# Optimization experiments

Measured on AMD Instinct MI355X. Metric: run time of the kernel, lower is better.

Reference implementation:

```python
import jax, jax.numpy as jnp
import numpy as np

N_NODES = 100000
HIDDEN = 64
N_LAYERS = 4
N_EDGES = 800000
EPS = 1e-5  # equinox RMSNorm default


def rmsnorm(x, w):
    # per-node RMSNorm over last dim, learned scale, no bias
    inv = jax.lax.rsqrt(jnp.mean(x * x, axis=-1, keepdims=True) + EPS)
    return x * inv * w


def setup_inputs() -> dict:
    key = jax.random.key(0)
    ks = jax.random.split(key, 5)
    x = jax.random.normal(ks[0], (N_NODES, HIDDEN), dtype=jnp.float32)
    # eqx Linear weight (out,in), init ~ U(-1/sqrt(in), 1/sqrt(in)); randn*scale is fine for a baseline
    scale = 1.0 / np.sqrt(HIDDEN)
    conv_w = jax.random.normal(ks[1], (N_LAYERS, HIDDEN, HIDDEN), dtype=jnp.float32) * scale
    hid_w = jax.random.normal(ks[2], (N_LAYERS, HIDDEN, HIDDEN), dtype=jnp.float32) * scale
    conv_norm_w = jnp.ones((N_LAYERS, HIDDEN), dtype=jnp.float32)
    hid_norm_w = jnp.ones((N_LAYERS, HIDDEN), dtype=jnp.float32)
    row = jax.random.randint(ks[3], (N_EDGES,), 0, N_NODES, dtype=jnp.int32)
    col = jax.random.randint(ks[4], (N_EDGES,), 0, N_NODES, dtype=jnp.int32)
    return {"x": x, "conv_w": conv_w, "conv_norm_w": conv_norm_w,
            "hid_w": hid_w, "hid_norm_w": hid_norm_w, "row": row, "col": col}


def reference(x, conv_w, conv_norm_w, hid_w, hid_norm_w, row, col):
    n_nodes = x.shape[0]

    def step(h, params):
        cw, cnw, hw, hnw = params
        # GConvLayer: linear (no bias) -> relu -> sparse adjacency aggregation -> residual RMSNorm
        m = jax.nn.relu(h @ cw.T)                                  # [n_nodes, d]
        agg = jax.ops.segment_sum(m[col], row, num_segments=n_nodes)  # a @ m (unweighted COO)
        h = rmsnorm(h + agg, cnw)
        # HiddenLayer: linear -> relu -> residual RMSNorm
        y = jax.nn.relu(h @ hw.T)
        h = rmsnorm(h + y, hnw)
        return h, None

    x, _ = jax.lax.scan(step, x, (conv_w, conv_norm_w, hid_w, hid_norm_w))
    return x
```

## Files before the change

kernel.cpp:

```cpp
#include <hip/hip_runtime.h>
#include <hip/hip_bf16.h>

#define HIDDEN 64
#define EPS 1e-5f
#define NPB 64
#define WST 72

typedef __attribute__((ext_vector_type(8))) short bf16x8;
typedef __attribute__((ext_vector_type(4))) float f32x4;

__device__ __forceinline__ unsigned short f2b(float x) {
    __hip_bfloat16 b = __float2bfloat16(x);
    return *(unsigned short*)&b;
}
__device__ __forceinline__ float b2f(unsigned short u) {
    unsigned int ui = (unsigned int)u << 16;
    return *(float*)&ui;
}
__device__ __forceinline__ float b2f_lo(unsigned int u) { unsigned int ui = u << 16; return *(float*)&ui; }
__device__ __forceinline__ float b2f_hi(unsigned int u) { unsigned int ui = u & 0xffff0000u; return *(float*)&ui; }
__device__ __forceinline__ unsigned int pk2(float a, float b) {
    return (unsigned int)f2b(a) | ((unsigned int)f2b(b) << 16);
}


__global__ __launch_bounds__(256) void hist_rank_kernel(const int* __restrict__ row,
                                                        int* __restrict__ cnt,
                                                        int* __restrict__ erank, int e) {
    int stride = gridDim.x * blockDim.x;
    for (int i = blockIdx.x * blockDim.x + threadIdx.x; i < e; i += stride) {
        int r = row[i];
        erank[i] = atomicAdd(&cnt[r], 1);
    }
}

__global__ __launch_bounds__(256) void block_sum_kernel(const int* __restrict__ cnt,
                                                        int* __restrict__ bsum, int n) {
    __shared__ int wsum[4];
    int tid = threadIdx.x;
    int i = blockIdx.x * 256 + tid;
    int v = (i < n) ? cnt[i] : 0;
#pragma unroll
    for (int off = 32; off > 0; off >>= 1) v += __shfl_xor(v, off, 64);
    if ((tid & 63) == 0) wsum[tid >> 6] = v;
    __syncthreads();
    if (tid == 0) bsum[blockIdx.x] = wsum[0] + wsum[1] + wsum[2] + wsum[3];
}

__global__ __launch_bounds__(256) void scan_final_kernel(const int* __restrict__ cnt,
                                                         const int* __restrict__ bsum,
                                                         int* __restrict__ row_ptr,
                                                         int n, int nb) {
    __shared__ int wred[4];
    __shared__ int wsum[4];
    __shared__ int wexcl[4];
    __shared__ int s_prev;
    __shared__ int s_tot;
    int b = blockIdx.x;
    int tid = threadIdx.x;
    int lane = tid & 63;
    int w = tid >> 6;
    int acc = 0;
    for (int j = tid; j < b; j += 256) acc += bsum[j];
#pragma unroll
    for (int off = 32; off > 0; off >>= 1) acc += __shfl_xor(acc, off, 64);
    if (lane == 0) wred[w] = acc;
    int i = b * 256 + tid;
    int v = (i < n) ? cnt[i] : 0;
    int sc = v;
#pragma unroll
    for (int off = 1; off < 64; off <<= 1) {
        int t = __shfl_up(sc, off, 64);
        if (lane >= off) sc += t;
    }
    if (lane == 63) wsum[w] = sc;
    __syncthreads();
    if (tid == 0) {
        s_prev = wred[0] + wred[1] + wred[2] + wred[3];
        int a = 0;
#pragma unroll
        for (int j = 0; j < 4; j++) { wexcl[j] = a; a += wsum[j]; }
        s_tot = a;
    }
    __syncthreads();
    if (i < n) row_ptr[i] = s_prev + wexcl[w] + (sc - v);
    if (b == nb - 1 && tid == 0) row_ptr[n] = s_prev + s_tot;
}

__global__ __launch_bounds__(256) void fill_kernel(const int* __restrict__ row,
                                                   const int* __restrict__ col,
                                                   const int* __restrict__ row_ptr,
                                                   const int* __restrict__ erank,
                                                   int* __restrict__ ecol, int e, int n) {
    int cls = blockIdx.x & 7;
    int sub = blockIdx.x >> 3;
    int nsub = gridDim.x >> 3;
    int lo = (int)(((long long)n * cls) >> 3);
    int hi = (int)(((long long)n * (cls + 1)) >> 3);
    for (int i = sub * 256 + threadIdx.x; i < e; i += nsub * 256) {
        int r = row[i];
        if (r >= lo && r < hi) {
            int pos = row_ptr[r] + erank[i];
            ecol[pos] = col[i];
        }
    }
}

__global__ __launch_bounds__(256) void wconv_kernel(const float* __restrict__ cw,
                                                    const float* __restrict__ hw,
                                                    unsigned short* __restrict__ wbt, int L) {
    int idx = blockIdx.x * blockDim.x + threadIdx.x;
    int total = 2 * L * 4096;
    if (idx >= total) return;
    int mat = idx >> 12;
    int rem = idx & 4095;
    const float* src = (mat < L) ? (cw + (size_t)mat * 4096) : (hw + (size_t)(mat - L) * 4096);
    wbt[idx] = f2b(src[rem]);
}


__device__ __forceinline__ void mfma_tile(const unsigned short* s_a,
                                          const unsigned short* s_b,
                                          int l16, int quad, int wbase, f32x4 acc[4]) {
    const unsigned short* ap = &s_a[(size_t)(wbase + l16) * WST + quad * 8];
    const unsigned short* bp = &s_b[(size_t)l16 * WST + quad * 8];
#pragma unroll
    for (int kt = 0; kt < 2; kt++) {
        bf16x8 a = *(const bf16x8*)(ap + kt * 32);
#pragma unroll
        for (int nt = 0; nt < 4; nt++) {
            bf16x8 b = *(const bf16x8*)(bp + (size_t)nt * 16 * WST + kt * 32);
            acc[nt] = __builtin_amdgcn_mfma_f32_16x16x32_bf16(a, b, acc[nt], 0, 0, 0);
        }
    }
}

__device__ __forceinline__ void stage_wb(const unsigned short* __restrict__ wsrc,
                                         unsigned short* s_wb, int tid) {
    for (int i = tid; i < 512; i += 256) {
        int r = i >> 3, seg = i & 7;
        *(uint4*)(&s_wb[r * WST + seg * 8]) = ((const uint4*)(wsrc + r * 64))[seg];
    }
}

__device__ __forceinline__ void acc8(float* p, uint4 u, bool ok) {
    p[0] += ok ? b2f_lo(u.x) : 0.f;
    p[1] += ok ? b2f_hi(u.x) : 0.f;
    p[2] += ok ? b2f_lo(u.y) : 0.f;
    p[3] += ok ? b2f_hi(u.y) : 0.f;
    p[4] += ok ? b2f_lo(u.z) : 0.f;
    p[5] += ok ? b2f_hi(u.z) : 0.f;
    p[6] += ok ? b2f_lo(u.w) : 0.f;
    p[7] += ok ? b2f_hi(u.w) : 0.f;
}


__global__ __launch_bounds__(256) void mm_relu_kernel(const float* __restrict__ h,
                                                      const unsigned short* __restrict__ wb,
                                                      __hip_bfloat16* __restrict__ m, int n) {
    __shared__ unsigned short s_hb[NPB * WST];
    __shared__ unsigned short s_wb[64 * WST];
    int tid = threadIdx.x;
    int base = blockIdx.x * NPB;
    stage_wb(wb, s_wb, tid);
    for (int i = tid; i < 512; i += 256) {
        int r = i >> 3, seg = i & 7;
        if (base + r < n) {
            const float4* hp = (const float4*)(h + (size_t)(base + r) * HIDDEN + seg * 8);
            float4 ha = hp[0], hb = hp[1];
            uint4 p;
            p.x = pk2(ha.x, ha.y);
            p.y = pk2(ha.z, ha.w);
            p.z = pk2(hb.x, hb.y);
            p.w = pk2(hb.z, hb.w);
            *(uint4*)(&s_hb[r * WST + seg * 8]) = p;
        } else {
            *(uint4*)(&s_hb[r * WST + seg * 8]) = make_uint4(0u, 0u, 0u, 0u);
        }
    }
    __syncthreads();
    int lane = tid & 63, wave = tid >> 6;
    int quad = lane >> 4, l16 = lane & 15;
    int wbase = wave * 16;
    f32x4 acc[4];
    acc[0] = (f32x4){0.f,0.f,0.f,0.f}; acc[1] = (f32x4){0.f,0.f,0.f,0.f};
    acc[2] = (f32x4){0.f,0.f,0.f,0.f}; acc[3] = (f32x4){0.f,0.f,0.f,0.f};
    mfma_tile(s_hb, s_wb, l16, quad, wbase, acc);
    unsigned short* mo = (unsigned short*)m;
#pragma unroll
    for (int r = 0; r < 4; r++) {
        int node = base + wbase + quad * 4 + r;
        if (node < n) {
#pragma unroll
            for (int nt = 0; nt < 4; nt++)
                mo[(size_t)node * HIDDEN + nt * 16 + l16] = f2b(fmaxf(acc[nt][r], 0.f));
        }
    }
}


__global__ __launch_bounds__(256) void fused_layer_kernel(
        const float* hf, const __hip_bfloat16* hb_in,
        const __hip_bfloat16* __restrict__ m_in,
        const unsigned short* __restrict__ hwb,
        const unsigned short* cwb_next,
        const int* __restrict__ row_ptr, const int* __restrict__ ecol,
        const float* __restrict__ cnw, const float* __restrict__ hnw,
        float* out_f32, __hip_bfloat16* hb_new, __hip_bfloat16* m_out, int n) {
    __shared__ unsigned short s_hb[NPB * WST];
    __shared__ unsigned short s_wb[64 * WST];
    int tid = threadIdx.x;
    int base = blockIdx.x * NPB;
    int lane = tid & 63, wave = tid >> 6;

    stage_wb(hwb, s_wb, tid);

    int g = lane >> 2;
    int sl = lane & 3;
    int gb = lane & ~3;
    int nl = wave * 16 + g;
    int node = base + nl;

    const float4* cp = (const float4*)(cnw + 16 * sl);
    float4 c0 = cp[0], c1 = cp[1], c2 = cp[2], c3 = cp[3];
    const unsigned short* mi = (const unsigned short*)m_in;

    uint4 q0 = make_uint4(0u, 0u, 0u, 0u);
    uint4 q1 = make_uint4(0u, 0u, 0u, 0u);
    if (node < n) {
        float p[16];
        if (hf) {
            const float4* hp = (const float4*)(hf + (size_t)node * HIDDEN + 16 * sl);
            float4 v0 = hp[0], v1 = hp[1], v2 = hp[2], v3 = hp[3];
            p[0]=v0.x;  p[1]=v0.y;  p[2]=v0.z;  p[3]=v0.w;
            p[4]=v1.x;  p[5]=v1.y;  p[6]=v1.z;  p[7]=v1.w;
            p[8]=v2.x;  p[9]=v2.y;  p[10]=v2.z; p[11]=v2.w;
            p[12]=v3.x; p[13]=v3.y; p[14]=v3.z; p[15]=v3.w;
        } else {
            const uint4* hp = (const uint4*)((const unsigned short*)hb_in + (size_t)node * HIDDEN + 16 * sl);
            uint4 u0 = hp[0], u1 = hp[1];
            p[0]=b2f_lo(u0.x);  p[1]=b2f_hi(u0.x);
            p[2]=b2f_lo(u0.y);  p[3]=b2f_hi(u0.y);
            p[4]=b2f_lo(u0.z);  p[5]=b2f_hi(u0.z);
            p[6]=b2f_lo(u0.w);  p[7]=b2f_hi(u0.w);
            p[8]=b2f_lo(u1.x);  p[9]=b2f_hi(u1.x);
            p[10]=b2f_lo(u1.y); p[11]=b2f_hi(u1.y);
            p[12]=b2f_lo(u1.z); p[13]=b2f_hi(u1.z);
            p[14]=b2f_lo(u1.w); p[15]=b2f_hi(u1.w);
        }
        int beg = row_ptr[node];
        int end = row_ptr[node + 1];
        int myc = 0;
        if (beg < end) {
            int idx = beg + sl;
            myc = ecol[idx < end ? idx : end - 1];
        }
        for (int b0 = beg; b0 < end; b0 += 4) {
            int nxt = b0 + 4;
            int nmyc = 0;
            if (nxt < end) {
                int idx = nxt + sl;
                nmyc = ecol[idx < end ? idx : end - 1];
            }
            int cnt = end - b0;
            if (cnt > 4) cnt = 4;
            int cj[4];
#pragma unroll
            for (int j = 0; j < 4; j++) cj[j] = __shfl(myc, gb + j, 64);
            uint4 ua[4], ub[4];
#pragma unroll
            for (int j = 0; j < 4; j++) {
                const uint4* mp = (const uint4*)(mi + (size_t)cj[j] * HIDDEN + 16 * sl);
                ua[j] = mp[0];
                ub[j] = mp[1];
            }
#pragma unroll
            for (int j = 0; j < 4; j++) {
                bool ok = j < cnt;
                acc8(p, ua[j], ok);
                acc8(p + 8, ub[j], ok);
            }
            myc = nmyc;
        }
        float ss = 0.f;
#pragma unroll
        for (int k = 0; k < 16; k++) ss += p[k] * p[k];
        ss += __shfl_xor(ss, 1, 64);
        ss += __shfl_xor(ss, 2, 64);
        float inv = rsqrtf(ss * (1.0f / 64.0f) + EPS);
        q0.x = pk2(p[0]*inv*c0.x,  p[1]*inv*c0.y);
        q0.y = pk2(p[2]*inv*c0.z,  p[3]*inv*c0.w);
        q0.z = pk2(p[4]*inv*c1.x,  p[5]*inv*c1.y);
        q0.w = pk2(p[6]*inv*c1.z,  p[7]*inv*c1.w);
        q1.x = pk2(p[8]*inv*c2.x,  p[9]*inv*c2.y);
        q1.y = pk2(p[10]*inv*c2.z, p[11]*inv*c2.w);
        q1.z = pk2(p[12]*inv*c3.x, p[13]*inv*c3.y);
        q1.w = pk2(p[14]*inv*c3.z, p[15]*inv*c3.w);
    }
    *(uint4*)(&s_hb[(size_t)nl * WST + 16 * sl]) = q0;
    *(uint4*)(&s_hb[(size_t)nl * WST + 16 * sl + 8]) = q1;
    __syncthreads();

    int quad = lane >> 4, l16 = lane & 15;
    int wbase = wave * 16;
    f32x4 acc[4];
    acc[0] = (f32x4){0.f,0.f,0.f,0.f}; acc[1] = (f32x4){0.f,0.f,0.f,0.f};
    acc[2] = (f32x4){0.f,0.f,0.f,0.f}; acc[3] = (f32x4){0.f,0.f,0.f,0.f};
    mfma_tile(s_hb, s_wb, l16, quad, wbase, acc);

    float hv[4][4];
    float ssq[4] = {0.f, 0.f, 0.f, 0.f};
#pragma unroll
    for (int r = 0; r < 4; r++) {
        int nr = wbase + quad * 4 + r;
#pragma unroll
        for (int nt = 0; nt < 4; nt++) {
            float hres = b2f(s_hb[(size_t)nr * WST + nt * 16 + l16]);
            float v = hres + fmaxf(acc[nt][r], 0.f);
            hv[r][nt] = v;
            ssq[r] += v * v;
        }
    }
#pragma unroll
    for (int mk = 1; mk <= 8; mk <<= 1) {
#pragma unroll
        for (int r = 0; r < 4; r++) ssq[r] += __shfl_xor(ssq[r], mk, 64);
    }
    float nwv[4];
#pragma unroll
    for (int nt = 0; nt < 4; nt++) nwv[nt] = hnw[nt * 16 + l16];
#pragma unroll
    for (int r = 0; r < 4; r++) {
        float inv = rsqrtf(ssq[r] * (1.0f / 64.0f) + EPS);
#pragma unroll
        for (int nt = 0; nt < 4; nt++) hv[r][nt] *= inv * nwv[nt];
    }
    if (out_f32) {
#pragma unroll
        for (int r = 0; r < 4; r++) {
            int nd = base + wbase + quad * 4 + r;
            if (nd < n) {
#pragma unroll
                for (int nt = 0; nt < 4; nt++)
                    out_f32[(size_t)nd * HIDDEN + nt * 16 + l16] = hv[r][nt];
            }
        }
    }
    if (hb_new) {
        unsigned short* ho = (unsigned short*)hb_new;
#pragma unroll
        for (int r = 0; r < 4; r++) {
            int nd = base + wbase + quad * 4 + r;
            if (nd < n) {
#pragma unroll
                for (int nt = 0; nt < 4; nt++)
                    ho[(size_t)nd * HIDDEN + nt * 16 + l16] = f2b(hv[r][nt]);
            }
        }
    }

    if (!m_out) return;

    bf16x8 wf[8];
    {
        const unsigned short* wp = cwb_next + (size_t)l16 * 64 + quad * 8;
#pragma unroll
        for (int nt = 0; nt < 4; nt++) {
#pragma unroll
            for (int kt = 0; kt < 2; kt++)
                wf[nt * 2 + kt] = *(const bf16x8*)(wp + (size_t)nt * 16 * 64 + kt * 32);
        }
    }

#pragma unroll
    for (int r = 0; r < 4; r++) {
        int nr = wbase + quad * 4 + r;
#pragma unroll
        for (int nt = 0; nt < 4; nt++)
            s_hb[(size_t)nr * WST + nt * 16 + l16] = f2b(hv[r][nt]);
    }

    f32x4 acc2[4];
    acc2[0] = (f32x4){0.f,0.f,0.f,0.f}; acc2[1] = (f32x4){0.f,0.f,0.f,0.f};
    acc2[2] = (f32x4){0.f,0.f,0.f,0.f}; acc2[3] = (f32x4){0.f,0.f,0.f,0.f};
    {
        const unsigned short* ap = &s_hb[(size_t)(wbase + l16) * WST + quad * 8];
#pragma unroll
        for (int kt = 0; kt < 2; kt++) {
            bf16x8 a = *(const bf16x8*)(ap + kt * 32);
#pragma unroll
            for (int nt = 0; nt < 4; nt++)
                acc2[nt] = __builtin_amdgcn_mfma_f32_16x16x32_bf16(a, wf[nt * 2 + kt], acc2[nt], 0, 0, 0);
        }
    }
    unsigned short* mo = (unsigned short*)m_out;
#pragma unroll
    for (int r = 0; r < 4; r++) {
        int nd = base + wbase + quad * 4 + r;
        if (nd < n) {
#pragma unroll
            for (int nt = 0; nt < 4; nt++)
                mo[(size_t)nd * HIDDEN + nt * 16 + l16] = f2b(fmaxf(acc2[nt][r], 0.f));
        }
    }
}


static inline size_t align_up(size_t x, size_t a) { return (x + a - 1) & ~(a - 1); }

extern "C" void kernel_launch(void* const* d_in, const int* in_sizes, int n_in,
                              void* d_out, int out_size, void* d_ws, size_t ws_size,
                              hipStream_t stream) {
    const float* x       = (const float*)d_in[0];
    const float* conv_w  = (const float*)d_in[1];
    const float* conv_nw = (const float*)d_in[2];
    const float* hid_w   = (const float*)d_in[3];
    const float* hid_nw  = (const float*)d_in[4];
    const int*   row     = (const int*)d_in[5];
    const int*   col     = (const int*)d_in[6];
    float* out = (float*)d_out;

    const int n = in_sizes[0] / HIDDEN;
    const int e = in_sizes[5];
    const int L = in_sizes[1] / 4096;

    size_t off = 0;
    char* ws = (char*)d_ws;
    __hip_bfloat16* mA = (__hip_bfloat16*)(ws + off);  off = align_up(off + (size_t)n * HIDDEN * 2, 16);
    __hip_bfloat16* mB = (__hip_bfloat16*)(ws + off);  off = align_up(off + (size_t)n * HIDDEN * 2, 16);
    __hip_bfloat16* hb1 = (__hip_bfloat16*)(ws + off); off = align_up(off + (size_t)n * HIDDEN * 2, 16);
    __hip_bfloat16* hb2 = (__hip_bfloat16*)(ws + off); off = align_up(off + (size_t)n * HIDDEN * 2, 16);
    unsigned short* wbt = (unsigned short*)(ws + off); off = align_up(off + (size_t)2 * L * 4096 * 2, 16);
    int* row_ptr = (int*)(ws + off);           off = align_up(off + (size_t)(n + 1) * 4, 16);
    int* cnt = (int*)(ws + off);               off = align_up(off + (size_t)n * 4, 16);
    int* bsum = (int*)(ws + off);              off = align_up(off + (size_t)1024 * 4, 16);
    int* erank = (int*)(ws + off);             off = align_up(off + (size_t)e * 4, 16);
    int* ecol = (int*)(ws + off);              off = align_up(off + (size_t)e * 4, 16);

    const int nb = (n + 255) / 256;

    hipMemsetAsync(cnt, 0, (size_t)n * 4, stream);
    hist_rank_kernel<<<1024, 256, 0, stream>>>(row, cnt, erank, e);
    block_sum_kernel<<<nb, 256, 0, stream>>>(cnt, bsum, n);
    scan_final_kernel<<<nb, 256, 0, stream>>>(cnt, bsum, row_ptr, n, nb);
    fill_kernel<<<1024, 256, 0, stream>>>(row, col, row_ptr, erank, ecol, e, n);

    wconv_kernel<<<(2 * L * 4096 + 255) / 256, 256, 0, stream>>>(conv_w, hid_w, wbt, L);

    const int blocks = (n + NPB - 1) / NPB;

    mm_relu_kernel<<<blocks, 256, 0, stream>>>(x, wbt, mA, n);

    const __hip_bfloat16* mi = mA;
    __hip_bfloat16* mo = mB;
    __hip_bfloat16* hin = nullptr;
    __hip_bfloat16* hout = hb1;
    for (int l = 0; l < L; l++) {
        bool last = (l == L - 1);
        fused_layer_kernel<<<blocks, 256, 0, stream>>>(
            (l == 0) ? x : nullptr, hin, mi,
            wbt + (size_t)(L + l) * 4096,
            last ? nullptr : (wbt + (size_t)(l + 1) * 4096),
            row_ptr, ecol,
            conv_nw + (size_t)l * HIDDEN, hid_nw + (size_t)l * HIDDEN,
            last ? out : nullptr,
            last ? nullptr : hout,
            last ? nullptr : mo, n);
        __hip_bfloat16* tmp = (__hip_bfloat16*)mi; mi = mo; mo = tmp;
        hin = hout;
        hout = (hout == hb1) ? hb2 : hb1;
    }
}
```

Before: 291.0 us.

## Drop LDS weight staging and block barrier; use 128-thread blocks in fused layer

Measured after the change: 291.9 us. No clear change (+0.3%).

```diff
diff --git a/kernel.cpp b/kernel.cpp
--- a/kernel.cpp
+++ b/kernel.cpp
@@ -4,6 +4,7 @@
 #define HIDDEN 64
 #define EPS 1e-5f
 #define NPB 64
+#define FNPB 32
 #define WST 72
 
 typedef __attribute__((ext_vector_type(8))) short bf16x8;
@@ -132,6 +133,17 @@
             bf16x8 b = *(const bf16x8*)(bp + (size_t)nt * 16 * WST + kt * 32);
             acc[nt] = __builtin_amdgcn_mfma_f32_16x16x32_bf16(a, b, acc[nt], 0, 0, 0);
         }
+    }
+}
+
+__device__ __forceinline__ void load_wfrag(const unsigned short* __restrict__ w,
+                                           int l16, int quad, bf16x8 wf[8]) {
+    const unsigned short* wp = w + (size_t)l16 * 64 + quad * 8;
+#pragma unroll
+    for (int nt = 0; nt < 4; nt++) {
+#pragma unroll
+        for (int kt = 0; kt < 2; kt++)
+            wf[nt * 2 + kt] = *(const bf16x8*)(wp + (size_t)nt * 16 * 64 + kt * 32);
     }
 }
 
@@ -199,7 +211,7 @@
 }
 
 
-__global__ __launch_bounds__(256) void fused_layer_kernel(
+__global__ __launch_bounds__(128, 6) void fused_layer_kernel(
         const float* hf, const __hip_bfloat16* hb_in,
         const __hip_bfloat16* __restrict__ m_in,
         const unsigned short* __restrict__ hwb,
@@ -207,13 +219,10 @@
         const int* __restrict__ row_ptr, const int* __restrict__ ecol,
         const float* __restrict__ cnw, const float* __restrict__ hnw,
         float* out_f32, __hip_bfloat16* hb_new, __hip_bfloat16* m_out, int n) {
-    __shared__ unsigned short s_hb[NPB * WST];
-    __shared__ unsigned short s_wb[64 * WST];
+    __shared__ unsigned short s_hb[FNPB * WST];
     int tid = threadIdx.x;
-    int base = blockIdx.x * NPB;
+    int base = blockIdx.x * FNPB;
     int lane = tid & 63, wave = tid >> 6;
-
-    stage_wb(hwb, s_wb, tid);
 
     int g = lane >> 2;
     int sl = lane & 3;
@@ -221,8 +230,6 @@
     int nl = wave * 16 + g;
     int node = base + nl;
 
-    const float4* cp = (const float4*)(cnw + 16 * sl);
-    float4 c0 = cp[0], c1 = cp[1], c2 = cp[2], c3 = cp[3];
     const unsigned short* mi = (const unsigned short*)m_in;
 
     uint4 q0 = make_uint4(0u, 0u, 0u, 0u);
@@ -288,6 +295,8 @@
         ss += __shfl_xor(ss, 1, 64);
         ss += __shfl_xor(ss, 2, 64);
         float inv = rsqrtf(ss * (1.0f / 64.0f) + EPS);
+        const float4* cp = (const float4*)(cnw + 16 * sl);
+        float4 c0 = cp[0], c1 = cp[1], c2 = cp[2], c3 = cp[3];
         q0.x = pk2(p[0]*inv*c0.x,  p[1]*inv*c0.y);
         q0.y = pk2(p[2]*inv*c0.z,  p[3]*inv*c0.w);
         q0.z = pk2(p[4]*inv*c1.x,  p[5]*inv*c1.y);
@@ -299,14 +308,24 @@
     }
     *(uint4*)(&s_hb[(size_t)nl * WST + 16 * sl]) = q0;
     *(uint4*)(&s_hb[(size_t)nl * WST + 16 * sl + 8]) = q1;
-    __syncthreads();
 
     int quad = lane >> 4, l16 = lane & 15;
     int wbase = wave * 16;
+    bf16x8 wfh[8];
+    load_wfrag(hwb, l16, quad, wfh);
     f32x4 acc[4];
     acc[0] = (f32x4){0.f,0.f,0.f,0.f}; acc[1] = (f32x4){0.f,0.f,0.f,0.f};
     acc[2] = (f32x4){0.f,0.f,0.f,0.f}; acc[3] = (f32x4){0.f,0.f,0.f,0.f};
-    mfma_tile(s_hb, s_wb, l16, quad, wbase, acc);
+    {
+        const unsigned short* ap = &s_hb[(size_t)(wbase + l16) * WST + quad * 8];
+#pragma unroll
+        for (int kt = 0; kt < 2; kt++) {
+            bf16x8 a = *(const bf16x8*)(ap + kt * 32);
+#pragma unroll
+            for (int nt = 0; nt < 4; nt++)
+                acc[nt] = __builtin_amdgcn_mfma_f32_16x16x32_bf16(a, wfh[nt * 2 + kt], acc[nt], 0, 0, 0);
+        }
+    }
 
     float hv[4][4];
     float ssq[4] = {0.f, 0.f, 0.f, 0.f};
@@ -326,6 +345,8 @@
 #pragma unroll
         for (int r = 0; r < 4; r++) ssq[r] += __shfl_xor(ssq[r], mk, 64);
     }
+    bf16x8 wfc[8];
+    if (m_out) load_wfrag(cwb_next, l16, quad, wfc);
     float nwv[4];
 #pragma unroll
     for (int nt = 0; nt < 4; nt++) nwv[nt] = hnw[nt * 16 + l16];
@@ -360,17 +381,6 @@
     }
 
     if (!m_out) return;
-
-    bf16x8 wf[8];
-    {
-        const unsigned short* wp = cwb_next + (size_t)l16 * 64 + quad * 8;
-#pragma unroll
-        for (int nt = 0; nt < 4; nt++) {
-#pragma unroll
-            for (int kt = 0; kt < 2; kt++)
-                wf[nt * 2 + kt] = *(const bf16x8*)(wp + (size_t)nt * 16 * 64 + kt * 32);
-        }
-    }
 
 #pragma unroll
     for (int r = 0; r < 4; r++) {
@@ -390,7 +400,7 @@
             bf16x8 a = *(const bf16x8*)(ap + kt * 32);
 #pragma unroll
             for (int nt = 0; nt < 4; nt++)
-                acc2[nt] = __builtin_amdgcn_mfma_f32_16x16x32_bf16(a, wf[nt * 2 + kt], acc2[nt], 0, 0, 0);
+                acc2[nt] = __builtin_amdgcn_mfma_f32_16x16x32_bf16(a, wfc[nt * 2 + kt], acc2[nt], 0, 0, 0);
         }
     }
     unsigned short* mo = (unsigned short*)m_out;
@@ -447,17 +457,16 @@
 
     wconv_kernel<<<(2 * L * 4096 + 255) / 256, 256, 0, stream>>>(conv_w, hid_w, wbt, L);
 
-    const int blocks = (n + NPB - 1) / NPB;
-
-    mm_relu_kernel<<<blocks, 256, 0, stream>>>(x, wbt, mA, n);
-
+    mm_relu_kernel<<<(n + NPB - 1) / NPB, 256, 0, stream>>>(x, wbt, mA, n);
+
+    const int fblocks = (n + FNPB - 1) / FNPB;
     const __hip_bfloat16* mi = mA;
     __hip_bfloat16* mo = mB;
     __hip_bfloat16* hin = nullptr;
     __hip_bfloat16* hout = hb1;
     for (int l = 0; l < L; l++) {
         bool last = (l == L - 1);
-        fused_layer_kernel<<<blocks, 256, 0, stream>>>(
+        fused_layer_kernel<<<fblocks, 128, 0, stream>>>(
             (l == 0) ? x : nullptr, hin, mi,
             wbt + (size_t)(L + l) * 4096,
             last ? nullptr : (wbt + (size_t)(l + 1) * 4096),
```
